# Optimization experiments

Measured on AMD Instinct MI355X. Metric: run time of the kernel, lower is better.

Reference implementation:

```python
import jax, jax.numpy as jnp
import numpy as np

HID = 2048; H = 16; QLR = 1536; KVLR = 512
DN = 128; DR = 64; DV = 128; DQ = DN + DR  # 192
B = 2; S = 2048
THETA = 10000.0; EPS = 1e-6


def rms_norm(x, w, eps=EPS):
    x32 = x.astype(jnp.float32)
    var = jnp.mean(x32 * x32, axis=-1, keepdims=True)
    return (w * (x32 * jax.lax.rsqrt(var + eps))).astype(x.dtype)


def rotate_half(x):
    x1, x2 = jnp.split(x, 2, axis=-1)
    return jnp.concatenate((-x2, x1), axis=-1)


def rope_tables(seq_len, dim, base=THETA):
    inv_freq = 1.0 / (base ** (jnp.arange(0, dim, 2, dtype=jnp.float32) / dim))
    t = jnp.arange(seq_len, dtype=jnp.float32)
    freqs = jnp.outer(t, inv_freq)            # [S, dim/2]
    emb = jnp.concatenate((freqs, freqs), -1)  # [S, dim]
    return jnp.cos(emb), jnp.sin(emb)


def setup_inputs() -> dict:
    key = jax.random.key(0)
    ks = jax.random.split(key, 8)
    sd = lambda fan_in: 1.0 / np.sqrt(fan_in)
    return {
        "hidden_states": jax.random.normal(ks[0], (B, S, HID), jnp.float32),
        "w_qa": jax.random.normal(ks[1], (QLR, HID), jnp.float32) * sd(HID),
        "q_a_ln_w": jnp.ones((QLR,), jnp.float32),
        "w_qb": jax.random.normal(ks[2], (H * DQ, QLR), jnp.float32) * sd(QLR),
        "w_kva": jax.random.normal(ks[3], (KVLR + DR, HID), jnp.float32) * sd(HID),
        "kv_a_ln_w": jnp.ones((KVLR,), jnp.float32),
        "w_kvb": jax.random.normal(ks[4], (H * (DN + DV), KVLR), jnp.float32) * sd(KVLR),
        "w_o": jax.random.normal(ks[5], (HID, H * DV), jnp.float32) * sd(H * DV),
    }


def reference(hidden_states, w_qa, q_a_ln_w, w_qb, w_kva, kv_a_ln_w, w_kvb, w_o):
    b, s, _ = hidden_states.shape
    scale = DQ ** -0.5
    cos, sin = rope_tables(s, DR)  # [S, DR] each

    # Q path: low-rank down-proj -> RMSNorm -> up-proj
    cq = rms_norm(hidden_states @ w_qa.T, q_a_ln_w)            # [B,S,QLR]
    q = (cq @ w_qb.T).reshape(b, s, H, DQ).transpose(0, 2, 1, 3)  # [B,H,S,DQ]
    q_nope, q_pe = q[..., :DN], q[..., DN:]
    q_pe = q_pe * cos + rotate_half(q_pe) * sin

    # KV path: joint compressed kv + shared rope key
    ckv = hidden_states @ w_kva.T                               # [B,S,KVLR+DR]
    k_pe = ckv[..., KVLR:].reshape(b, s, 1, DR).transpose(0, 2, 1, 3)  # [B,1,S,DR]
    k_pe = k_pe * cos + rotate_half(k_pe) * sin
    ckv_l = rms_norm(ckv[..., :KVLR], kv_a_ln_w)                # [B,S,KVLR]
    kv = (ckv_l @ w_kvb.T).reshape(b, s, H, DN + DV).transpose(0, 2, 1, 3)
    k_nope, v = kv[..., :DN], kv[..., DN:]                      # [B,H,S,DN],[B,H,S,DV]

    q_full = jnp.concatenate([q_nope, q_pe], axis=-1)           # [B,H,S,DQ]
    k_full = jnp.concatenate(
        [k_nope, jnp.broadcast_to(k_pe, (b, H, s, DR))], axis=-1)

    scores = jnp.einsum('bhqd,bhkd->bhqk', q_full, k_full) * scale
    causal = jnp.triu(jnp.ones((s, s), dtype=bool), k=1)
    scores = jnp.where(causal, -jnp.inf, scores)
    attn = jax.nn.softmax(scores.astype(jnp.float32), axis=-1).astype(q_full.dtype)

    out = jnp.einsum('bhqk,bhkd->bhqd', attn, v)                # [B,H,S,DV]
    out = out.transpose(0, 2, 1, 3).reshape(b, s, H * DV)
    return out @ w_o.T
```

## Files before the change

kernel.cpp:

```cpp
#include <hip/hip_runtime.h>
#include <stdint.h>
#include <stddef.h>

typedef unsigned short u16;
typedef short s16x8 __attribute__((ext_vector_type(8)));
typedef unsigned short u16x4 __attribute__((ext_vector_type(4)));
typedef unsigned short u16x8 __attribute__((ext_vector_type(8)));
typedef float f32x4 __attribute__((ext_vector_type(4)));

__device__ __forceinline__ u16 f2b(float f) {
  uint32_t u = __builtin_bit_cast(uint32_t, f);
  uint32_t r = u + 0x7fffu + ((u >> 16) & 1u);
  return (u16)(r >> 16);
}
__device__ __forceinline__ float b2f(u16 h) {
  uint32_t u = ((uint32_t)h) << 16;
  return __builtin_bit_cast(float, u);
}
__device__ __forceinline__ void gl_lds16(const void* g, void* l) {
  __builtin_amdgcn_global_load_lds((const __attribute__((address_space(1))) void*)g,
                                   (__attribute__((address_space(3))) void*)l,
                                   16, 0, 0);
}

__global__ __launch_bounds__(256) void cast_k(const float* __restrict__ in,
                                              u16* __restrict__ out, int n4) {
  int i = blockIdx.x * 256 + threadIdx.x;
  if (i >= n4) return;
  float4 v = ((const float4*)in)[i];
  u16x4 o; o[0]=f2b(v.x); o[1]=f2b(v.y); o[2]=f2b(v.z); o[3]=f2b(v.w);
  ((u16x4*)out)[i] = o;
}

__global__ __launch_bounds__(256) void cast_pad_k(const float* __restrict__ in,
                                                  u16* __restrict__ out,
                                                  int Kd, int nvalid, int n4) {
  int i = blockIdx.x * 256 + threadIdx.x;
  if (i >= n4) return;
  int row = (i << 2) / Kd;
  u16x4 o;
  if (row < nvalid) {
    float4 v = ((const float4*)in)[i];
    o[0]=f2b(v.x); o[1]=f2b(v.y); o[2]=f2b(v.z); o[3]=f2b(v.w);
  } else {
    o[0]=0; o[1]=0; o[2]=0; o[3]=0;
  }
  ((u16x4*)out)[i] = o;
}

template<int OUT_BF16>
__global__ __launch_bounds__(256) void gemm_bt(const u16* __restrict__ A,
                                               const u16* __restrict__ B,
                                               void* __restrict__ Cv,
                                               int M, int N, int K) {
  __shared__ u16 As[128 * 32];
  __shared__ u16 Bs[128 * 32];
  const int t = threadIdx.x;
  const int w = t >> 6, l = t & 63;
  const int nb = N >> 7;
  const int cpx = gridDim.x >> 3;
  const int swz = (blockIdx.x & 7) * cpx + (blockIdx.x >> 3);
  const int bm = (swz / nb) << 7;
  const int bn = (swz % nb) << 7;
  const int wr = (w >> 1) << 6;
  const int wc = (w & 1) << 6;

  f32x4 acc[4][4];
  #pragma unroll
  for (int i = 0; i < 4; i++)
    #pragma unroll
    for (int j = 0; j < 4; j++) acc[i][j] = (f32x4){0.f, 0.f, 0.f, 0.f};

  const u16* ga = A + (size_t)(bm + w * 32 + (l >> 2)) * K + ((l & 3) * 8);
  const u16* gb = B + (size_t)(bn + w * 32 + (l >> 2)) * K + ((l & 3) * 8);
  u16* la0 = &As[(w * 32) * 32];
  u16* la1 = &As[(w * 32 + 16) * 32];
  u16* lb0 = &Bs[(w * 32) * 32];
  u16* lb1 = &Bs[(w * 32 + 16) * 32];

  for (int k0 = 0; k0 < K; k0 += 32) {
    __syncthreads();
    gl_lds16(ga, la0);
    gl_lds16(ga + (size_t)16 * K, la1);
    gl_lds16(gb, lb0);
    gl_lds16(gb + (size_t)16 * K, lb1);
    ga += 32; gb += 32;
    __syncthreads();

    s16x8 af[4], bf[4];
    #pragma unroll
    for (int i = 0; i < 4; i++) {
      af[i] = *(const s16x8*)&As[(wr + i * 16 + (l & 15)) * 32 + (l >> 4) * 8];
      bf[i] = *(const s16x8*)&Bs[(wc + i * 16 + (l & 15)) * 32 + (l >> 4) * 8];
    }
    #pragma unroll
    for (int mi = 0; mi < 4; mi++)
      #pragma unroll
      for (int ni = 0; ni < 4; ni++)
        acc[mi][ni] = __builtin_amdgcn_mfma_f32_16x16x32_bf16(af[mi], bf[ni], acc[mi][ni], 0, 0, 0);
  }

  #pragma unroll
  for (int mi = 0; mi < 4; mi++)
    #pragma unroll
    for (int ni = 0; ni < 4; ni++) {
      int row0 = bm + wr + mi * 16 + ((l >> 4) << 2);
      int col  = bn + wc + ni * 16 + (l & 15);
      #pragma unroll
      for (int r = 0; r < 4; r++) {
        float v = acc[mi][ni][r];
        if (OUT_BF16) ((u16*)Cv)[(size_t)(row0 + r) * N + col] = f2b(v);
        else          ((float*)Cv)[(size_t)(row0 + r) * N + col] = v;
      }
    }
}

__global__ __launch_bounds__(256) void rmsnorm_k(const float* __restrict__ X,
                                                 const float* __restrict__ W,
                                                 u16* __restrict__ Y, int ldx, int D) {
  const int row = blockIdx.x;
  const float* x = X + (size_t)row * ldx;
  const int t = threadIdx.x;
  float ss = 0.f;
  for (int i = t; i < (D >> 2); i += 256) {
    float4 v = ((const float4*)x)[i];
    ss += v.x * v.x + v.y * v.y + v.z * v.z + v.w * v.w;
  }
  #pragma unroll
  for (int off = 32; off > 0; off >>= 1) ss += __shfl_xor(ss, off);
  __shared__ float red[4];
  if ((t & 63) == 0) red[t >> 6] = ss;
  __syncthreads();
  float tot = red[0] + red[1] + red[2] + red[3];
  float r = rsqrtf(tot / (float)D + 1e-6f);
  u16* y = Y + (size_t)row * D;
  for (int i = t; i < (D >> 2); i += 256) {
    float4 v = ((const float4*)x)[i];
    float4 g = ((const float4*)W)[i];
    u16x4 o;
    o[0] = f2b(v.x * r * g.x); o[1] = f2b(v.y * r * g.y);
    o[2] = f2b(v.z * r * g.z); o[3] = f2b(v.w * r * g.w);
    ((u16x4*)y)[i] = o;
  }
}

__global__ __launch_bounds__(256) void rope_kpe_k(const float* __restrict__ CKV,
                                                  u16* __restrict__ Kpe) {
  int idx = blockIdx.x * 256 + threadIdx.x;
  if (idx >= 4096 * 32) return;
  int d = idx & 31;
  int m = idx >> 5;
  int s = m & 2047;
  float inv = expf(-(float)(2 * d) * (9.210340371976184f / 64.0f));
  float ang = (float)s * inv;
  float sn, c;
  sincosf(ang, &sn, &c);
  float x1 = CKV[(size_t)m * 640 + 512 + d];
  float x2 = CKV[(size_t)m * 640 + 544 + d];
  Kpe[m * 64 + d]      = f2b(x1 * c - x2 * sn);
  Kpe[m * 64 + 32 + d] = f2b(x2 * c + x1 * sn);
}

__global__ __launch_bounds__(256) void rope_q_k(u16* __restrict__ Qb) {
  int idx = blockIdx.x * 256 + threadIdx.x;
  if (idx >= 4096 * 16 * 32) return;
  int d = idx & 31;
  int h = (idx >> 5) & 15;
  int m = idx >> 9;
  int s = m & 2047;
  float inv = expf(-(float)(2 * d) * (9.210340371976184f / 64.0f));
  float ang = (float)s * inv;
  float sn, c;
  sincosf(ang, &sn, &c);
  size_t base = (size_t)m * 3072 + h * 192 + 128 + d;
  float x1 = b2f(Qb[base]);
  float x2 = b2f(Qb[base + 32]);
  Qb[base]      = f2b(x1 * c - x2 * sn);
  Qb[base + 32] = f2b(x2 * c + x1 * sn);
}

__global__ __launch_bounds__(256) void vt_k(const u16* __restrict__ KV,
                                            u16* __restrict__ VT) {
  __shared__ u16 L[64][72];
  const int t = threadIdx.x;
  const int s_t = blockIdx.x & 31;
  const int d_t = (blockIdx.x >> 5) & 1;
  const int bh  = blockIdx.x >> 6;
  const int h = bh & 15, b = bh >> 4;
  const size_t bS = (size_t)b * 2048;
  const int s0 = s_t << 6, d0 = d_t << 6;

  #pragma unroll
  for (int i = 0; i < 2; i++) {
    int rs = (t >> 3) + i * 32;
    int ch = t & 7;
    u16x8 v = *(const u16x8*)&KV[(bS + s0 + rs) * 4096 + h * 256 + 128 + d0 + ch * 8];
    *(u16x8*)&L[rs][ch * 8] = v;
  }
  __syncthreads();
  #pragma unroll
  for (int i = 0; i < 2; i++) {
    int rd = (t >> 3) + i * 32;
    int ch = t & 7;
    u16x8 o;
    #pragma unroll
    for (int j = 0; j < 8; j++) o[j] = L[ch * 8 + j][rd];
    *(u16x8*)&VT[((size_t)bh * 128 + d0 + rd) * 2048 + s0 + ch * 8] = o;
  }
}

__global__ __launch_bounds__(256) void attn3_k(const u16* __restrict__ Q,
                                               const u16* __restrict__ KV,
                                               const u16* __restrict__ Kpe,
                                               const u16* __restrict__ VT,
                                               u16* __restrict__ O) {
  const float SCALE = 0.07216878364870322f;
  const int t = threadIdx.x, w = t >> 6, l = t & 63;
  const int bh = blockIdx.x & 31;
  const int qt = 31 - (blockIdx.x >> 5);
  const int h = bh & 15, b = bh >> 4;
  const int q0 = qt << 6;
  const size_t bS = (size_t)b * 2048;

  __shared__ u16 Kl[2][64 * 192];
  __shared__ u16 Pl[4][16][72];

  s16x8 qf[6];
  {
    const u16* qp = Q + (bS + q0 + w * 16 + (l & 15)) * 3072 + h * 192 + ((l >> 4) * 8);
    #pragma unroll
    for (int c = 0; c < 6; c++) qf[c] = *(const s16x8*)(qp + c * 32);
  }
  float m_i[4] = {-1e30f, -1e30f, -1e30f, -1e30f};
  float lp[4]  = {0.f, 0.f, 0.f, 0.f};
  f32x4 accO[8];
  #pragma unroll
  for (int i = 0; i < 8; i++) accO[i] = (f32x4){0.f, 0.f, 0.f, 0.f};

  const u16* vbp = VT + (size_t)bh * 128 * 2048;
  const int ktiles = qt + 1;

  auto STAGE = [&](int buf, int k0) {
    #pragma unroll
    for (int it = 0; it < 6; ++it) {
      int sl = it * 64 + l;
      int r = w * 16 + sl / 24;
      int cc = (sl % 24) ^ (r & 7);
      const u16* src = (cc < 16)
          ? KV + (bS + k0 + r) * 4096 + h * 256 + cc * 8
          : Kpe + (bS + k0 + r) * 64 + (cc - 16) * 8;
      gl_lds16(src, &Kl[buf][w * 3072 + it * 512]);
    }
  };

  STAGE(0, 0);
  __syncthreads();

  int cur = 0;
  for (int kt = 0; kt < ktiles; ++kt) {
    const int k0 = kt << 6;
    if (kt + 1 < ktiles) STAGE(cur ^ 1, k0 + 64);

    s16x8 va[8], vb[8];
    #pragma unroll
    for (int df = 0; df < 8; df++)
      va[df] = *(const s16x8*)&vbp[(size_t)(df * 16 + (l & 15)) * 2048 + k0 + (l >> 4) * 8];
    #pragma unroll
    for (int df = 0; df < 8; df++)
      vb[df] = *(const s16x8*)&vbp[(size_t)(df * 16 + (l & 15)) * 2048 + k0 + 32 + (l >> 4) * 8];

    f32x4 sa[4];
    #pragma unroll
    for (int cf = 0; cf < 4; cf++) sa[cf] = (f32x4){0.f, 0.f, 0.f, 0.f};
    #pragma unroll
    for (int c = 0; c < 6; c++) {
      #pragma unroll
      for (int cf = 0; cf < 4; cf++) {
        int row = cf * 16 + (l & 15);
        int ch = (c * 4 + (l >> 4)) ^ (row & 7);
        s16x8 kf = *(const s16x8*)&Kl[cur][row * 192 + ch * 8];
        sa[cf] = __builtin_amdgcn_mfma_f32_16x16x32_bf16(qf[c], kf, sa[cf], 0, 0, 0);
      }
    }

    const bool diag = (kt == qt);
    #pragma unroll
    for (int cf = 0; cf < 4; cf++)
      #pragma unroll
      for (int r = 0; r < 4; r++) {
        float s = sa[cf][r] * SCALE;
        if (diag) {
          int qrow = q0 + w * 16 + ((l >> 4) << 2) + r;
          if (k0 + cf * 16 + (l & 15) > qrow) s = -1e30f;
        }
        sa[cf][r] = s;
      }

    float lm[4];
    #pragma unroll
    for (int r = 0; r < 4; r++)
      lm[r] = fmaxf(fmaxf(sa[0][r], sa[1][r]), fmaxf(sa[2][r], sa[3][r]));
    bool safe = (lm[0] <= m_i[0] + 8.f) && (lm[1] <= m_i[1] + 8.f) &&
                (lm[2] <= m_i[2] + 8.f) && (lm[3] <= m_i[3] + 8.f);
    if (!__all(safe)) {
      #pragma unroll
      for (int r = 0; r < 4; r++) {
        float mx = lm[r];
        #pragma unroll
        for (int dd = 1; dd < 16; dd <<= 1) mx = fmaxf(mx, __shfl_xor(mx, dd));
        float mnew = fmaxf(m_i[r], mx);
        float alpha = __expf(m_i[r] - mnew);
        m_i[r] = mnew;
        lp[r] *= alpha;
        #pragma unroll
        for (int df = 0; df < 8; df++) accO[df][r] *= alpha;
      }
    }
    #pragma unroll
    for (int r = 0; r < 4; r++) {
      float e0 = __expf(sa[0][r] - m_i[r]);
      float e1 = __expf(sa[1][r] - m_i[r]);
      float e2 = __expf(sa[2][r] - m_i[r]);
      float e3 = __expf(sa[3][r] - m_i[r]);
      lp[r] += (e0 + e1) + (e2 + e3);
      int prow = ((l >> 4) << 2) + r;
      Pl[w][prow][(l & 15)]      = f2b(e0);
      Pl[w][prow][16 + (l & 15)] = f2b(e1);
      Pl[w][prow][32 + (l & 15)] = f2b(e2);
      Pl[w][prow][48 + (l & 15)] = f2b(e3);
    }

    {
      s16x8 pf0 = *(const s16x8*)&Pl[w][l & 15][(l >> 4) * 8];
      #pragma unroll
      for (int df = 0; df < 8; df++)
        accO[df] = __builtin_amdgcn_mfma_f32_16x16x32_bf16(pf0, va[df], accO[df], 0, 0, 0);
      s16x8 pf1 = *(const s16x8*)&Pl[w][l & 15][32 + (l >> 4) * 8];
      #pragma unroll
      for (int df = 0; df < 8; df++)
        accO[df] = __builtin_amdgcn_mfma_f32_16x16x32_bf16(pf1, vb[df], accO[df], 0, 0, 0);
    }

    __syncthreads();
    cur ^= 1;
  }

  #pragma unroll
  for (int r = 0; r < 4; r++) {
    float s = lp[r];
    #pragma unroll
    for (int dd = 1; dd < 16; dd <<= 1) s += __shfl_xor(s, dd);
    float rl = 1.0f / s;
    #pragma unroll
    for (int df = 0; df < 8; df++) {
      float o = accO[df][r] * rl;
      O[(bS + q0 + w * 16 + ((l >> 4) << 2) + r) * 2048 + h * 128 + df * 16 + (l & 15)] = f2b(o);
    }
  }
}

extern "C" void kernel_launch(void* const* d_in, const int* in_sizes, int n_in,
                              void* d_out, int out_size, void* d_ws, size_t ws_size,
                              hipStream_t stream) {
  const float* hs    = (const float*)d_in[0];
  const float* w_qa  = (const float*)d_in[1];
  const float* q_ln  = (const float*)d_in[2];
  const float* w_qb  = (const float*)d_in[3];
  const float* w_kva = (const float*)d_in[4];
  const float* kv_ln = (const float*)d_in[5];
  const float* w_kvb = (const float*)d_in[6];
  const float* w_o   = (const float*)d_in[7];
  float* out = (float*)d_out;

  char* ws = (char*)d_ws;
  size_t off = 0;
  auto alloc = [&](size_t bytes) -> void* {
    void* p = ws + off;
    off = (off + bytes + 255) & ~(size_t)255;
    return p;
  };
  u16* Xb     = (u16*)alloc(4096ull * 2048 * 2);
  u16* Wqa    = (u16*)alloc(1536ull * 2048 * 2);
  u16* Wqb    = (u16*)alloc(3072ull * 1536 * 2);
  u16* Wkva   = (u16*)alloc(640ull * 2048 * 2);
  u16* Wkvb   = (u16*)alloc(4096ull * 512 * 2);
  u16* Wo     = (u16*)alloc(2048ull * 2048 * 2);
  float* CQraw = (float*)alloc(4096ull * 1536 * 4);
  float* CKV   = (float*)alloc(4096ull * 640 * 4);
  u16* CQn    = (u16*)alloc(4096ull * 1536 * 2);
  u16* CKVn   = (u16*)alloc(4096ull * 512 * 2);
  u16* Kpe    = (u16*)alloc(4096ull * 64 * 2);
  u16* KVb    = (u16*)alloc(4096ull * 4096 * 2);
  u16* Ob     = (u16*)alloc(4096ull * 2048 * 2);
  u16* Qb     = (u16*)CQraw;
  u16* VT     = Xb;

  cast_k<<<dim3(8388608 / 4 / 256), 256, 0, stream>>>(hs, Xb, 8388608 / 4);
  cast_k<<<dim3(3145728 / 4 / 256), 256, 0, stream>>>(w_qa, Wqa, 3145728 / 4);
  cast_k<<<dim3(4718592 / 4 / 256), 256, 0, stream>>>(w_qb, Wqb, 4718592 / 4);
  cast_pad_k<<<dim3(1310720 / 4 / 256), 256, 0, stream>>>(w_kva, Wkva, 2048, 576, 1310720 / 4);
  cast_k<<<dim3(2097152 / 4 / 256), 256, 0, stream>>>(w_kvb, Wkvb, 2097152 / 4);
  cast_k<<<dim3(4194304 / 4 / 256), 256, 0, stream>>>(w_o, Wo, 4194304 / 4);

  gemm_bt<0><<<dim3(32 * 12), 256, 0, stream>>>(Xb, Wqa, CQraw, 4096, 1536, 2048);
  gemm_bt<0><<<dim3(32 * 5), 256, 0, stream>>>(Xb, Wkva, CKV, 4096, 640, 2048);

  rmsnorm_k<<<dim3(4096), 256, 0, stream>>>(CQraw, q_ln, CQn, 1536, 1536);
  rmsnorm_k<<<dim3(4096), 256, 0, stream>>>(CKV, kv_ln, CKVn, 640, 512);
  rope_kpe_k<<<dim3(4096 * 32 / 256), 256, 0, stream>>>(CKV, Kpe);

  gemm_bt<1><<<dim3(32 * 24), 256, 0, stream>>>(CQn, Wqb, Qb, 4096, 3072, 1536);
  gemm_bt<1><<<dim3(32 * 32), 256, 0, stream>>>(CKVn, Wkvb, KVb, 4096, 4096, 512);
  rope_q_k<<<dim3(4096 * 16 * 32 / 256), 256, 0, stream>>>(Qb);

  vt_k<<<dim3(32 * 2 * 32), 256, 0, stream>>>(KVb, VT);

  attn3_k<<<dim3(32 * 32), 256, 0, stream>>>(Qb, KVb, Kpe, VT, Ob);

  gemm_bt<0><<<dim3(32 * 16), 256, 0, stream>>>(Ob, Wo, out, 4096, 2048, 2048);
}
```

Measured before the change: 561.6 us.

## Merge down-projection GEMMs, add split-K atomics, and reorder attention staging with priority hints

The q_a and kv_a weights are concatenated so one GEMM produces both compressed streams. That GEMM and the output projection now use split-K over two grid slices, accumulating with float atomics into buffers zeroed by memset. In the attention kernel, the next K tile is staged after the V loads are issued, and s_setprio raises wave priority around the MFMA blocks. The aim is fewer launches and better CU occupancy for the small-N GEMMs, at the cost of extra memsets, atomic traffic and nondeterministic summation order.

```diff
diff --git a/kernel.cpp b/kernel.cpp
--- a/kernel.cpp
+++ b/kernel.cpp
@@ -48,7 +48,7 @@
   ((u16x4*)out)[i] = o;
 }
 
-template<int OUT_BF16>
+template<int MODE>
 __global__ __launch_bounds__(256) void gemm_bt(const u16* __restrict__ A,
                                                const u16* __restrict__ B,
                                                void* __restrict__ Cv,
@@ -64,6 +64,8 @@
   const int bn = (swz % nb) << 7;
   const int wr = (w >> 1) << 6;
   const int wc = (w & 1) << 6;
+  const int Kh = K / gridDim.y;
+  const int ks0 = blockIdx.y * Kh;
 
   f32x4 acc[4][4];
   #pragma unroll
@@ -71,14 +73,14 @@
     #pragma unroll
     for (int j = 0; j < 4; j++) acc[i][j] = (f32x4){0.f, 0.f, 0.f, 0.f};
 
-  const u16* ga = A + (size_t)(bm + w * 32 + (l >> 2)) * K + ((l & 3) * 8);
-  const u16* gb = B + (size_t)(bn + w * 32 + (l >> 2)) * K + ((l & 3) * 8);
+  const u16* ga = A + (size_t)(bm + w * 32 + (l >> 2)) * K + ks0 + ((l & 3) * 8);
+  const u16* gb = B + (size_t)(bn + w * 32 + (l >> 2)) * K + ks0 + ((l & 3) * 8);
   u16* la0 = &As[(w * 32) * 32];
   u16* la1 = &As[(w * 32 + 16) * 32];
   u16* lb0 = &Bs[(w * 32) * 32];
   u16* lb1 = &Bs[(w * 32 + 16) * 32];
 
-  for (int k0 = 0; k0 < K; k0 += 32) {
+  for (int k0 = 0; k0 < Kh; k0 += 32) {
     __syncthreads();
     gl_lds16(ga, la0);
     gl_lds16(ga + (size_t)16 * K, la1);
@@ -109,8 +111,10 @@
       #pragma unroll
       for (int r = 0; r < 4; r++) {
         float v = acc[mi][ni][r];
-        if (OUT_BF16) ((u16*)Cv)[(size_t)(row0 + r) * N + col] = f2b(v);
-        else          ((float*)Cv)[(size_t)(row0 + r) * N + col] = v;
+        size_t idx = (size_t)(row0 + r) * N + col;
+        if (MODE == 1)      ((u16*)Cv)[idx] = f2b(v);
+        else if (MODE == 0) ((float*)Cv)[idx] = v;
+        else                atomicAdd((float*)Cv + idx, v);
       }
     }
 }
@@ -144,7 +148,7 @@
   }
 }
 
-__global__ __launch_bounds__(256) void rope_kpe_k(const float* __restrict__ CKV,
+__global__ __launch_bounds__(256) void rope_kpe_k(const float* __restrict__ CQ,
                                                   u16* __restrict__ Kpe) {
   int idx = blockIdx.x * 256 + threadIdx.x;
   if (idx >= 4096 * 32) return;
@@ -155,8 +159,8 @@
   float ang = (float)s * inv;
   float sn, c;
   sincosf(ang, &sn, &c);
-  float x1 = CKV[(size_t)m * 640 + 512 + d];
-  float x2 = CKV[(size_t)m * 640 + 544 + d];
+  float x1 = CQ[(size_t)m * 2176 + 2048 + d];
+  float x2 = CQ[(size_t)m * 2176 + 2080 + d];
   Kpe[m * 64 + d]      = f2b(x1 * c - x2 * sn);
   Kpe[m * 64 + 32 + d] = f2b(x2 * c + x1 * sn);
 }
@@ -209,7 +213,7 @@
   }
 }
 
-__global__ __launch_bounds__(256) void attn3_k(const u16* __restrict__ Q,
+__global__ __launch_bounds__(256) void attn4_k(const u16* __restrict__ Q,
                                                const u16* __restrict__ KV,
                                                const u16* __restrict__ Kpe,
                                                const u16* __restrict__ VT,
@@ -259,7 +263,6 @@
   int cur = 0;
   for (int kt = 0; kt < ktiles; ++kt) {
     const int k0 = kt << 6;
-    if (kt + 1 < ktiles) STAGE(cur ^ 1, k0 + 64);
 
     s16x8 va[8], vb[8];
     #pragma unroll
@@ -269,9 +272,12 @@
     for (int df = 0; df < 8; df++)
       vb[df] = *(const s16x8*)&vbp[(size_t)(df * 16 + (l & 15)) * 2048 + k0 + 32 + (l >> 4) * 8];
 
+    if (kt + 1 < ktiles) STAGE(cur ^ 1, k0 + 64);
+
     f32x4 sa[4];
     #pragma unroll
     for (int cf = 0; cf < 4; cf++) sa[cf] = (f32x4){0.f, 0.f, 0.f, 0.f};
+    __builtin_amdgcn_s_setprio(1);
     #pragma unroll
     for (int c = 0; c < 6; c++) {
       #pragma unroll
@@ -282,6 +288,7 @@
         sa[cf] = __builtin_amdgcn_mfma_f32_16x16x32_bf16(qf[c], kf, sa[cf], 0, 0, 0);
       }
     }
+    __builtin_amdgcn_s_setprio(0);
 
     const bool diag = (kt == qt);
     #pragma unroll
@@ -332,13 +339,15 @@
 
     {
       s16x8 pf0 = *(const s16x8*)&Pl[w][l & 15][(l >> 4) * 8];
+      s16x8 pf1 = *(const s16x8*)&Pl[w][l & 15][32 + (l >> 4) * 8];
+      __builtin_amdgcn_s_setprio(1);
       #pragma unroll
       for (int df = 0; df < 8; df++)
         accO[df] = __builtin_amdgcn_mfma_f32_16x16x32_bf16(pf0, va[df], accO[df], 0, 0, 0);
-      s16x8 pf1 = *(const s16x8*)&Pl[w][l & 15][32 + (l >> 4) * 8];
       #pragma unroll
       for (int df = 0; df < 8; df++)
         accO[df] = __builtin_amdgcn_mfma_f32_16x16x32_bf16(pf1, vb[df], accO[df], 0, 0, 0);
+      __builtin_amdgcn_s_setprio(0);
     }
 
     __syncthreads();
@@ -380,42 +389,41 @@
     return p;
   };
   u16* Xb     = (u16*)alloc(4096ull * 2048 * 2);
-  u16* Wqa    = (u16*)alloc(1536ull * 2048 * 2);
+  u16* Wcat   = (u16*)alloc(2176ull * 2048 * 2);
   u16* Wqb    = (u16*)alloc(3072ull * 1536 * 2);
-  u16* Wkva   = (u16*)alloc(640ull * 2048 * 2);
   u16* Wkvb   = (u16*)alloc(4096ull * 512 * 2);
   u16* Wo     = (u16*)alloc(2048ull * 2048 * 2);
-  float* CQraw = (float*)alloc(4096ull * 1536 * 4);
-  float* CKV   = (float*)alloc(4096ull * 640 * 4);
+  float* CQcat = (float*)alloc(4096ull * 2176 * 4);
   u16* CQn    = (u16*)alloc(4096ull * 1536 * 2);
   u16* CKVn   = (u16*)alloc(4096ull * 512 * 2);
   u16* Kpe    = (u16*)alloc(4096ull * 64 * 2);
   u16* KVb    = (u16*)alloc(4096ull * 4096 * 2);
   u16* Ob     = (u16*)alloc(4096ull * 2048 * 2);
-  u16* Qb     = (u16*)CQraw;
+  u16* Qb     = (u16*)CQcat;
   u16* VT     = Xb;
 
-  cast_k<<<dim3(8388608 / 4 / 256), 256, 0, stream>>>(hs, Xb, 8388608 / 4);
-  cast_k<<<dim3(3145728 / 4 / 256), 256, 0, stream>>>(w_qa, Wqa, 3145728 / 4);
-  cast_k<<<dim3(4718592 / 4 / 256), 256, 0, stream>>>(w_qb, Wqb, 4718592 / 4);
-  cast_pad_k<<<dim3(1310720 / 4 / 256), 256, 0, stream>>>(w_kva, Wkva, 2048, 576, 1310720 / 4);
-  cast_k<<<dim3(2097152 / 4 / 256), 256, 0, stream>>>(w_kvb, Wkvb, 2097152 / 4);
-  cast_k<<<dim3(4194304 / 4 / 256), 256, 0, stream>>>(w_o, Wo, 4194304 / 4);
-
-  gemm_bt<0><<<dim3(32 * 12), 256, 0, stream>>>(Xb, Wqa, CQraw, 4096, 1536, 2048);
-  gemm_bt<0><<<dim3(32 * 5), 256, 0, stream>>>(Xb, Wkva, CKV, 4096, 640, 2048);
-
-  rmsnorm_k<<<dim3(4096), 256, 0, stream>>>(CQraw, q_ln, CQn, 1536, 1536);
-  rmsnorm_k<<<dim3(4096), 256, 0, stream>>>(CKV, kv_ln, CKVn, 640, 512);
-  rope_kpe_k<<<dim3(4096 * 32 / 256), 256, 0, stream>>>(CKV, Kpe);
+  cast_k<<<dim3(8192), 256, 0, stream>>>(hs, Xb, 8388608 / 4);
+  cast_k<<<dim3(3072), 256, 0, stream>>>(w_qa, Wcat, 3145728 / 4);
+  cast_pad_k<<<dim3(1280), 256, 0, stream>>>(w_kva, Wcat + 1536ull * 2048, 2048, 576, 1310720 / 4);
+  cast_k<<<dim3(4608), 256, 0, stream>>>(w_qb, Wqb, 4718592 / 4);
+  cast_k<<<dim3(2048), 256, 0, stream>>>(w_kvb, Wkvb, 2097152 / 4);
+  cast_k<<<dim3(4096), 256, 0, stream>>>(w_o, Wo, 4194304 / 4);
+
+  hipMemsetAsync(CQcat, 0, 4096ull * 2176 * 4, stream);
+  gemm_bt<2><<<dim3(32 * 17, 2), 256, 0, stream>>>(Xb, Wcat, CQcat, 4096, 2176, 2048);
+
+  rmsnorm_k<<<dim3(4096), 256, 0, stream>>>(CQcat, q_ln, CQn, 2176, 1536);
+  rmsnorm_k<<<dim3(4096), 256, 0, stream>>>(CQcat + 1536, kv_ln, CKVn, 2176, 512);
+  rope_kpe_k<<<dim3(512), 256, 0, stream>>>(CQcat, Kpe);
 
   gemm_bt<1><<<dim3(32 * 24), 256, 0, stream>>>(CQn, Wqb, Qb, 4096, 3072, 1536);
   gemm_bt<1><<<dim3(32 * 32), 256, 0, stream>>>(CKVn, Wkvb, KVb, 4096, 4096, 512);
-  rope_q_k<<<dim3(4096 * 16 * 32 / 256), 256, 0, stream>>>(Qb);
+  rope_q_k<<<dim3(8192), 256, 0, stream>>>(Qb);
 
   vt_k<<<dim3(32 * 2 * 32), 256, 0, stream>>>(KVb, VT);
 
-  attn3_k<<<dim3(32 * 32), 256, 0, stream>>>(Qb, KVb, Kpe, VT, Ob);
-
-  gemm_bt<0><<<dim3(32 * 16), 256, 0, stream>>>(Ob, Wo, out, 4096, 2048, 2048);
-}
+  attn4_k<<<dim3(32 * 32), 256, 0, stream>>>(Qb, KVb, Kpe, VT, Ob);
+
+  hipMemsetAsync(out, 0, 4096ull * 2048 * 4, stream);
+  gemm_bt<2><<<dim3(32 * 16, 2), 256, 0, stream>>>(Ob, Wo, out, 4096, 2048, 2048);
+}
```

Result: slower. 623.7 us (+11.1%).
